# Optimization experiments

Hardware: AMD Instinct MI355X
Metric: run time of the kernel (lower is better)

The kernel has to match this reference:

```python
import jax, jax.numpy as jnp
import numpy as np

D_MODEL = 256
NUM_HEADS = 8
HEAD_DIM = D_MODEL // NUM_HEADS


def setup_inputs() -> dict:
    key = jax.random.key(0)
    ks = jax.random.split(key, 16)
    B, C, H, W = 2, D_MODEL, 64, 64
    s = 0.02
    inp = {
        "query_feat": jax.random.normal(ks[0], (B, C, H, W), jnp.float32),
        "lateral_feat": jax.random.normal(ks[1], (B, C, H, W), jnp.float32),
        # 1x1 convs == per-pixel linear layers: weight (out, in), bias (out,)
        "Wq": jax.random.normal(ks[2], (C, C), jnp.float32) * s,
        "bq": jnp.zeros((C,), jnp.float32),
        "Wk": jax.random.normal(ks[3], (C, C), jnp.float32) * s,
        "bk": jnp.zeros((C,), jnp.float32),
        "Wv": jax.random.normal(ks[4], (C, C), jnp.float32) * s,
        "bv": jnp.zeros((C,), jnp.float32),
        "Wo": jax.random.normal(ks[5], (C, C), jnp.float32) * s,
        "bo": jnp.zeros((C,), jnp.float32),
        "W1": jax.random.normal(ks[6], (4 * C, C), jnp.float32) * s,
        "b1": jnp.zeros((4 * C,), jnp.float32),
        "W2": jax.random.normal(ks[7], (C, 4 * C), jnp.float32) * s,
        "b2": jnp.zeros((C,), jnp.float32),
    }
    return inp


def reference(query_feat, lateral_feat, Wq, bq, Wk, bk, Wv, bv, Wo, bo, W1, b1, W2, b2):
    B, C, H, W = query_feat.shape
    N = H * W
    h, d = NUM_HEADS, HEAD_DIM
    scale = d ** -0.5

    # (B,C,H,W) -> (B,N,C) tokens
    xq = query_feat.reshape(B, C, N).transpose(0, 2, 1)
    xl = lateral_feat.reshape(B, C, N).transpose(0, 2, 1)

    # 1x1-conv projections = dense per-token linear
    Q = (xq @ Wq.T + bq).reshape(B, N, h, d).transpose(0, 2, 1, 3)  # (B,h,N,d)
    K = (xl @ Wk.T + bk).reshape(B, N, h, d).transpose(0, 2, 1, 3)
    V = (xl @ Wv.T + bv).reshape(B, N, h, d).transpose(0, 2, 1, 3)

    scores = jnp.einsum("bhqd,bhkd->bhqk", Q, K) * scale  # (B,h,N,N)
    attn = jax.nn.softmax(scores, axis=-1)  # dropout = identity at inference
    out = jnp.einsum("bhqk,bhkd->bhqd", attn, V)  # (B,h,N,d)

    out = out.transpose(0, 2, 1, 3).reshape(B, N, C)  # (B,N,C)
    out = out @ Wo.T + bo
    out = out.transpose(0, 2, 1).reshape(B, C, H, W)
    out = out + query_feat  # residual

    # MLP on channels (1x1 convs + exact GELU)
    t = out.reshape(B, C, N).transpose(0, 2, 1)  # (B,N,C)
    hdn = jax.nn.gelu(t @ W1.T + b1, approximate=False)  # (B,N,4C)
    mlp = (hdn @ W2.T + b2).transpose(0, 2, 1).reshape(B, C, H, W)
    return out + mlp
```

## Files before the change

### kernel.cpp

```cpp
#include <hip/hip_runtime.h>
#include <math.h>

namespace {

constexpr int kB  = 2;
constexpr int kC  = 256;
constexpr int kN  = 4096;
constexpr int kHD = 32;
constexpr int kC4 = 1024;

typedef __attribute__((ext_vector_type(8))) short bf16x8;
typedef __attribute__((ext_vector_type(4))) float f32x4;
typedef __attribute__((ext_vector_type(16))) float f32x16;

__device__ __forceinline__ float gelu_exact(float x) {
  return 0.5f * x * (1.0f + erff(x * 0.70710678118654752f));
}

__device__ __forceinline__ unsigned short f2bf(float x) {
  unsigned u = __builtin_bit_cast(unsigned, x);
  u += 0x7FFFu + ((u >> 16) & 1u);
  return (unsigned short)(u >> 16);
}

__device__ __forceinline__ float bf2f(unsigned short us) {
  return __builtin_bit_cast(float, (unsigned)us << 16);
}

__device__ __forceinline__ float exp2_hw(float x) {
#if __has_builtin(__builtin_amdgcn_exp2f)
  return __builtin_amdgcn_exp2f(x);
#else
  float r;
  asm("v_exp_f32 %0, %1\n\ts_nop 1" : "=v"(r) : "v"(x));
  return r;
#endif
}

__device__ __forceinline__ unsigned cvt_pk_bf16(float lo, float hi) {
  unsigned r;
  asm("v_cvt_pk_bf16_f32 %0, %1, %2" : "=v"(r) : "v"(lo), "v"(hi));
  return r;
}

__global__ __launch_bounds__(256)
void convert_all(const float* __restrict__ qfeat, const float* __restrict__ lfeat,
                 const float* __restrict__ Wq, const float* __restrict__ Wk,
                 const float* __restrict__ Wv, const float* __restrict__ Wo,
                 const float* __restrict__ W1, const float* __restrict__ W2,
                 unsigned short* __restrict__ qtok, unsigned short* __restrict__ ltok,
                 unsigned short* __restrict__ wbf)
{
  __shared__ float Lds[32][36];
  const int z = blockIdx.z;
  const int t = threadIdx.x;
  if (z < 4) {
    const float* src = (z < kB) ? qfeat : lfeat;
    unsigned short* dst = (z < kB) ? qtok : ltok;
    const int b = z & 1;
    src += (size_t)b * kC * kN;
    dst += (size_t)b * kN * kC;
    const int n0 = blockIdx.x * 32, c0 = blockIdx.y * 32;
    const int r = t >> 3, q4 = (t & 7) * 4;
    {
      const float4 v = *(const float4*)&src[(size_t)(c0 + r) * kN + n0 + q4];
      Lds[r][q4 + 0] = v.x; Lds[r][q4 + 1] = v.y; Lds[r][q4 + 2] = v.z; Lds[r][q4 + 3] = v.w;
    }
    __syncthreads();
    ushort4 p;
    p.x = f2bf(Lds[q4 + 0][r]); p.y = f2bf(Lds[q4 + 1][r]);
    p.z = f2bf(Lds[q4 + 2][r]); p.w = f2bf(Lds[q4 + 3][r]);
    *(ushort4*)&dst[(size_t)(n0 + r) * kC + c0 + q4] = p;
  } else {
    const int wi = blockIdx.y * 128 + blockIdx.x;
    if (wi >= 768) return;
    const int i4 = wi * 1024 + t * 4;
    const float* s; int base;
    if      (i4 < 65536)  { s = Wq; base = 0; }
    else if (i4 < 131072) { s = Wk; base = 65536; }
    else if (i4 < 196608) { s = Wv; base = 131072; }
    else if (i4 < 262144) { s = Wo; base = 196608; }
    else if (i4 < 524288) { s = W1; base = 262144; }
    else                  { s = W2; base = 524288; }
    const float4 v = *(const float4*)&s[i4 - base];
    ushort4 p;
    p.x = f2bf(v.x); p.y = f2bf(v.y); p.z = f2bf(v.z); p.w = f2bf(v.w);
    *(ushort4*)&wbf[i4] = p;
  }
}

template <int EPI, bool GELU, bool RES>
__global__ __launch_bounds__(256)
void gemm_mfma(const unsigned short* __restrict__ Wbf,
               const unsigned short* __restrict__ Xtok,
               const float* __restrict__ bias, const float* __restrict__ res,
               void* __restrict__ Y1, void* __restrict__ Y2,
               int M, int Nn, int K, float oscale)
{
  __shared__ unsigned short Wlds[64 * 64];
  __shared__ unsigned short Xlds[64 * 64];

  const int z = blockIdx.z;
  Xtok += (size_t)z * Nn * K;

  const int t = threadIdx.x;
  const int w = t >> 6, l = t & 63;
  const int r = l & 15, g = l >> 4;
  const int wm = w >> 1, wn = w & 1;
  const int m0 = blockIdx.y * 64, n0 = blockIdx.x * 64;

  const int rw = t >> 3;
  const int sw = (t & 7) ^ (rw & 7);
  const unsigned short* wsrc = Wbf + (size_t)(m0 + rw) * K + sw * 8;
  const unsigned short* xsrc = Xtok + (size_t)(n0 + rw) * K + sw * 8;

  f32x4 acc[2][2];
#pragma unroll
  for (int i = 0; i < 2; ++i)
#pragma unroll
    for (int j = 0; j < 2; ++j) acc[i][j] = {0.f, 0.f, 0.f, 0.f};

  bf16x8 wrg[2], xrg[2];
#pragma unroll
  for (int j = 0; j < 2; ++j) {
    wrg[j] = *(const bf16x8*)(wsrc + (size_t)(32 * j) * K);
    xrg[j] = *(const bf16x8*)(xsrc + (size_t)(32 * j) * K);
  }

  for (int k0 = 0; k0 < K; k0 += 64) {
    __syncthreads();
    *(bf16x8*)((char*)Wlds + t * 16)         = wrg[0];
    *(bf16x8*)((char*)Wlds + (256 + t) * 16) = wrg[1];
    *(bf16x8*)((char*)Xlds + t * 16)         = xrg[0];
    *(bf16x8*)((char*)Xlds + (256 + t) * 16) = xrg[1];
    __syncthreads();
    if (k0 + 64 < K) {
#pragma unroll
      for (int j = 0; j < 2; ++j) {
        wrg[j] = *(const bf16x8*)(wsrc + (size_t)(32 * j) * K + k0 + 64);
        xrg[j] = *(const bf16x8*)(xsrc + (size_t)(32 * j) * K + k0 + 64);
      }
    }
#pragma unroll
    for (int kc = 0; kc < 2; ++kc) {
      const int sl = ((kc * 4 + g) ^ (r & 7)) * 16;
      bf16x8 a0 = *(const bf16x8*)((const char*)Wlds + (wm * 32 + r) * 128 + sl);
      bf16x8 a1 = *(const bf16x8*)((const char*)Wlds + (wm * 32 + 16 + r) * 128 + sl);
      bf16x8 b0 = *(const bf16x8*)((const char*)Xlds + (wn * 32 + r) * 128 + sl);
      bf16x8 b1 = *(const bf16x8*)((const char*)Xlds + (wn * 32 + 16 + r) * 128 + sl);
      acc[0][0] = __builtin_amdgcn_mfma_f32_16x16x32_bf16(a0, b0, acc[0][0], 0, 0, 0);
      acc[0][1] = __builtin_amdgcn_mfma_f32_16x16x32_bf16(a0, b1, acc[0][1], 0, 0, 0);
      acc[1][0] = __builtin_amdgcn_mfma_f32_16x16x32_bf16(a1, b0, acc[1][0], 0, 0, 0);
      acc[1][1] = __builtin_amdgcn_mfma_f32_16x16x32_bf16(a1, b1, acc[1][1], 0, 0, 0);
    }
  }

#pragma unroll
  for (int f = 0; f < 2; ++f) {
    const int mb = m0 + wm * 32 + f * 16 + 4 * g;
    const float* bp = bias + mb;
    if constexpr (EPI == 4) { if (mb >= (M >> 1)) bp = res + (mb - (M >> 1)); }
    const float4 b4 = *(const float4*)bp;
#pragma unroll
    for (int fn = 0; fn < 2; ++fn) {
      const int n = n0 + wn * 32 + fn * 16 + r;
      float v[4];
      v[0] = (acc[f][fn][0] + b4.x) * oscale; v[1] = (acc[f][fn][1] + b4.y) * oscale;
      v[2] = (acc[f][fn][2] + b4.z) * oscale; v[3] = (acc[f][fn][3] + b4.w) * oscale;
      if (GELU) {
#pragma unroll
        for (int q = 0; q < 4; ++q) v[q] = gelu_exact(v[q]);
      }
      if (RES) {
#pragma unroll
        for (int q = 0; q < 4; ++q)
          v[q] += res[(size_t)z * M * Nn + (size_t)(mb + q) * Nn + n];
      }
      if constexpr (EPI == 1) {
        unsigned short* Yt = (unsigned short*)Y1 + (size_t)z * Nn * M;
        ushort4 pk;
        pk.x = f2bf(v[0]); pk.y = f2bf(v[1]); pk.z = f2bf(v[2]); pk.w = f2bf(v[3]);
        *(ushort4*)&Yt[(size_t)n * M + mb] = pk;
      }
      if constexpr (EPI == 4) {
        const int Mh = M >> 1;
        if (mb < Mh) {
          unsigned short* Yt = (unsigned short*)Y1 + (size_t)z * Nn * Mh;
          ushort4 pk;
          pk.x = f2bf(v[0]); pk.y = f2bf(v[1]); pk.z = f2bf(v[2]); pk.w = f2bf(v[3]);
          *(ushort4*)&Yt[(size_t)n * Mh + mb] = pk;
        } else {
          unsigned short* Yc = (unsigned short*)Y2 + (size_t)z * Mh * Nn;
#pragma unroll
          for (int q = 0; q < 4; ++q) Yc[(size_t)(mb - Mh + q) * Nn + n] = f2bf(v[q]);
        }
      }
      if constexpr (EPI == 6) {
        float* Yf = (float*)Y1 + (size_t)z * M * Nn;
        const unsigned short* Rt = (const unsigned short*)Y2 + (size_t)z * Nn * M;
#pragma unroll
        for (int q = 0; q < 4; ++q)
          Yf[(size_t)(mb + q) * Nn + n] = v[q] + bf2f(Rt[(size_t)n * M + mb + q]);
      }
    }
  }
}

__global__ __launch_bounds__(512, 4)
void attn_mfma32(const unsigned short* __restrict__ Qbf,
                 const unsigned short* __restrict__ Kbf,
                 const unsigned short* __restrict__ Vbf,
                 unsigned short* __restrict__ Aout)
{
  __shared__ __attribute__((aligned(16))) char smem[32768];

  const int id = blockIdx.x;
  const int bh = id & 15;
  const int b = bh >> 3, hd = bh & 7;
  const int t = threadIdx.x;
  const int w = t >> 6, l = t & 63;
  const int r = l & 31, hi = l >> 5;
  const int qg = w >> 1, kh = w & 1;

  const unsigned short* Qb = Qbf + (size_t)b * kN * kC;
  const unsigned short* Kb = Kbf + (size_t)b * kN * kC;
  const unsigned short* Vb = Vbf + ((size_t)b * kC + hd * kHD) * kN;
  unsigned short* Ap = Aout + (size_t)b * kN * kC;

  const int q0 = (id >> 4) * 128 + qg * 32;

  const bf16x8 qf0 = *(const bf16x8*)&Qb[(size_t)(q0 + r) * kC + hd * kHD + hi * 8];
  const bf16x8 qf1 = *(const bf16x8*)&Qb[(size_t)(q0 + r) * kC + hd * kHD + 16 + hi * 8];

  const int tt = t & 255, th = t >> 8;
  const unsigned short* ksrc = Kb + (size_t)(th * 2048 + (tt >> 2)) * kC + hd * kHD + (tt & 3) * 8;
  const unsigned short* vsrc = Vb + (size_t)(tt >> 3) * kN + th * 2048 + (tt & 7) * 8;
  char* kdst = smem + th * 4096 + ((tt & 3) * 64 + ((tt >> 2) ^ (9 * (tt & 3)))) * 16;
  char* vdst = smem + 8192 + th * 4096 + ((tt & 7) * 32 + ((tt >> 3) ^ (tt & 7))) * 16;

  int koff[2][2], voff[2][2];
#pragma unroll
  for (int ds = 0; ds < 2; ++ds)
#pragma unroll
    for (int tile = 0; tile < 2; ++tile) {
      const int c = 2 * ds + hi;
      koff[ds][tile] = kh * 4096 + (c * 64 + tile * 32 + (r ^ (9 * c))) * 16;
    }
#pragma unroll
  for (int ktile = 0; ktile < 2; ++ktile)
#pragma unroll
    for (int kc = 0; kc < 2; ++kc) {
      const int c = ktile * 4 + kc * 2 + hi;
      voff[ktile][kc] = 8192 + kh * 4096 + (c * 32 + (r ^ c)) * 16;
    }

  const f32x16 ZV = {0.f};
  f32x16 oA = ZV, oB = ZV;
  float lsum = 0.f;

  bf16x8 krg = *(const bf16x8*)ksrc;
  bf16x8 vrg = *(const bf16x8*)vsrc;

  for (int it = 0; it < 32; ++it) {
    const int bo = (it & 1) << 14;
    *(bf16x8*)(kdst + bo) = krg;
    *(bf16x8*)(vdst + bo) = vrg;
    if (it + 1 < 32) {
      krg = *(const bf16x8*)(ksrc + (size_t)(it + 1) * 64 * kC);
      vrg = *(const bf16x8*)(vsrc + (it + 1) * 64);
    }
    __syncthreads();

    bf16x8 ka00 = *(const bf16x8*)(smem + bo + koff[0][0]);
    bf16x8 ka10 = *(const bf16x8*)(smem + bo + koff[1][0]);
    bf16x8 ka01 = *(const bf16x8*)(smem + bo + koff[0][1]);
    bf16x8 ka11 = *(const bf16x8*)(smem + bo + koff[1][1]);
    __builtin_amdgcn_s_setprio(1);
    f32x16 s0 = __builtin_amdgcn_mfma_f32_32x32x16_bf16(ka00, qf0, ZV, 0, 0, 0);
    s0        = __builtin_amdgcn_mfma_f32_32x32x16_bf16(ka10, qf1, s0, 0, 0, 0);
    f32x16 s1 = __builtin_amdgcn_mfma_f32_32x32x16_bf16(ka01, qf0, ZV, 0, 0, 0);
    s1        = __builtin_amdgcn_mfma_f32_32x32x16_bf16(ka11, qf1, s1, 0, 0, 0);
    __builtin_amdgcn_s_setprio(0);

#pragma unroll
    for (int ktile = 0; ktile < 2; ++ktile) {
      const f32x16& sv = ktile ? s1 : s0;
      float pe[16];
#pragma unroll
      for (int j = 0; j < 16; ++j) pe[j] = exp2_hw(sv[j]);
      lsum += (((pe[0] + pe[1]) + (pe[2] + pe[3])) + ((pe[4] + pe[5]) + (pe[6] + pe[7])))
            + (((pe[8] + pe[9]) + (pe[10] + pe[11])) + ((pe[12] + pe[13]) + (pe[14] + pe[15])));
      const unsigned c0 = cvt_pk_bf16(pe[0], pe[1]),   c1 = cvt_pk_bf16(pe[2], pe[3]);
      const unsigned c2 = cvt_pk_bf16(pe[4], pe[5]),   c3 = cvt_pk_bf16(pe[6], pe[7]);
      const unsigned c4 = cvt_pk_bf16(pe[8], pe[9]),   c5 = cvt_pk_bf16(pe[10], pe[11]);
      const unsigned c6 = cvt_pk_bf16(pe[12], pe[13]), c7 = cvt_pk_bf16(pe[14], pe[15]);
      auto a02 = __builtin_amdgcn_permlane32_swap(c0, c2, false, false);
      auto a13 = __builtin_amdgcn_permlane32_swap(c1, c3, false, false);
      auto a46 = __builtin_amdgcn_permlane32_swap(c4, c6, false, false);
      auto a57 = __builtin_amdgcn_permlane32_swap(c5, c7, false, false);
      union { unsigned u[4]; bf16x8 v; } p0, p1;
      p0.u[0] = a02[0]; p0.u[1] = a13[0]; p0.u[2] = a02[1]; p0.u[3] = a13[1];
      p1.u[0] = a46[0]; p1.u[1] = a57[0]; p1.u[2] = a46[1]; p1.u[3] = a57[1];
      bf16x8 vf0 = *(const bf16x8*)(smem + bo + voff[ktile][0]);
      bf16x8 vf1 = *(const bf16x8*)(smem + bo + voff[ktile][1]);
      __builtin_amdgcn_s_setprio(1);
      oA = __builtin_amdgcn_mfma_f32_32x32x16_bf16(vf0, p0.v, oA, 0, 0, 0);
      oB = __builtin_amdgcn_mfma_f32_32x32x16_bf16(vf1, p1.v, oB, 0, 0, 0);
      __builtin_amdgcn_s_setprio(0);
    }
  }

  {
    auto pr = __builtin_amdgcn_permlane32_swap(
        __builtin_bit_cast(unsigned, lsum), __builtin_bit_cast(unsigned, lsum), false, false);
    lsum = __builtin_bit_cast(float, (unsigned)pr[0]) + __builtin_bit_cast(float, (unsigned)pr[1]);
  }
  float oS[16];
#pragma unroll
  for (int j = 0; j < 16; ++j) oS[j] = oA[j] + oB[j];

  float* Scr = (float*)smem;
  __syncthreads();
  if (kh == 1) {
    float* S = Scr + ((size_t)qg * 64 + l) * 17;
#pragma unroll
    for (int j = 0; j < 16; ++j) S[j] = oS[j];
    S[16] = lsum;
  }
  __syncthreads();
  if (kh == 0) {
    const float* S = Scr + ((size_t)qg * 64 + l) * 17;
#pragma unroll
    for (int j = 0; j < 16; ++j) oS[j] += S[j];
    lsum += S[16];
    const float inv = 1.f / lsum;

    unsigned* T = (unsigned*)(Scr + (size_t)qg * 64 * 17);
#pragma unroll
    for (int p = 0; p < 8; ++p) {
      const int r2 = 4 * (p >> 1) + 2 * hi + (p & 1);
      T[r2 * 33 + r] = cvt_pk_bf16(oS[2 * p] * inv, oS[2 * p + 1] * inv);
    }
    unsigned v[8];
#pragma unroll
    for (int j = 0; j < 8; ++j) v[j] = T[(8 * hi + j) * 33 + r];
    unsigned short* outp = Ap + (size_t)(q0 + r) * kC + hd * kHD + hi * 16;
    uint4 w0{v[0], v[1], v[2], v[3]}, w1{v[4], v[5], v[6], v[7]};
    *(uint4*)outp = w0;
    *(uint4*)(outp + 8) = w1;
  }
}

}

extern "C" void kernel_launch(void* const* d_in, const int* in_sizes, int n_in,
                              void* d_out, int out_size, void* d_ws, size_t ws_size,
                              hipStream_t stream)
{
  const float* qfeat = (const float*)d_in[0];
  const float* lfeat = (const float*)d_in[1];
  const float* Wq = (const float*)d_in[2];
  const float* bq = (const float*)d_in[3];
  const float* Wk = (const float*)d_in[4];
  const float* bk = (const float*)d_in[5];
  const float* Wv = (const float*)d_in[6];
  const float* bv = (const float*)d_in[7];
  const float* Wo = (const float*)d_in[8];
  const float* bo = (const float*)d_in[9];
  const float* W1 = (const float*)d_in[10];
  const float* b1 = (const float*)d_in[11];
  const float* W2 = (const float*)d_in[12];
  const float* b2 = (const float*)d_in[13];
  float* out = (float*)d_out;
  (void)in_sizes; (void)n_in; (void)out_size; (void)ws_size;

  constexpr float kScaleLog2e = 0.25506970f;

  const size_t bcn = (size_t)kB * kC * kN;
  unsigned short* qtok   = (unsigned short*)d_ws;
  unsigned short* ltok   = qtok + bcn;
  unsigned short* wbf    = ltok + bcn;
  unsigned short* qbf    = wbf + 786432;
  unsigned short* kbf    = qbf + bcn;
  unsigned short* vbf    = kbf + bcn;
  unsigned short* atok   = vbf + bcn;
  unsigned short* owstok = atok + bcn;
  unsigned short* h1tok  = owstok + bcn;

  dim3 blk(256);

  convert_all<<<dim3(128, 8, 5), blk, 0, stream>>>(
      qfeat, lfeat, Wq, Wk, Wv, Wo, W1, W2, qtok, ltok, wbf);

  gemm_mfma<1, false, false><<<dim3(64, 4, 2), blk, 0, stream>>>(
      wbf, qtok, bq, nullptr, qbf, nullptr, kC, kN, kC, kScaleLog2e);
  gemm_mfma<4, false, false><<<dim3(64, 8, 2), blk, 0, stream>>>(
      wbf + 65536, ltok, bk, bv, kbf, vbf, 2 * kC, kN, kC, 1.0f);

  attn_mfma32<<<dim3(512), dim3(512), 0, stream>>>(qbf, kbf, vbf, atok);

  gemm_mfma<1, false, true><<<dim3(64, 4, 2), blk, 0, stream>>>(
      wbf + 196608, atok, bo, qfeat, owstok, nullptr, kC, kN, kC, 1.0f);
  gemm_mfma<1, true, false><<<dim3(64, 16, 2), blk, 0, stream>>>(
      wbf + 262144, owstok, b1, nullptr, h1tok, nullptr, kC4, kN, kC, 1.0f);
  gemm_mfma<6, false, false><<<dim3(64, 4, 2), blk, 0, stream>>>(
      wbf + 524288, h1tok, b2, nullptr, out, owstok, kC, kN, kC4, 1.0f);
}
```

Measured before the change: 103.7 us.

## Software-pipeline attention loop: overlap next QK MFMA with current softmax-PV

The attention inner loop is restructured so that the QK^T MFMA for the next key tile is issued before the exp/PV work for the current tile, using two sets of score accumulators and a 4-stage LDS ring (LDS grows from 32KB to 64KB). The goal is to hide exp and permlane latency behind matrix-core work. The cost is higher register pressure from the extra score tiles, and the doubled shared memory may cut how many blocks fit per CU under the launch bound of 4.

```diff
diff --git a/kernel.cpp b/kernel.cpp
--- a/kernel.cpp
+++ b/kernel.cpp
@@ -212,7 +212,7 @@
                  const unsigned short* __restrict__ Vbf,
                  unsigned short* __restrict__ Aout)
 {
-  __shared__ __attribute__((aligned(16))) char smem[32768];
+  __shared__ __attribute__((aligned(16))) char smem[65536];
 
   const int id = blockIdx.x;
   const int bh = id & 15;
@@ -258,33 +258,27 @@
   f32x16 oA = ZV, oB = ZV;
   float lsum = 0.f;
 
-  bf16x8 krg = *(const bf16x8*)ksrc;
-  bf16x8 vrg = *(const bf16x8*)vsrc;
-
-  for (int it = 0; it < 32; ++it) {
-    const int bo = (it & 1) << 14;
-    *(bf16x8*)(kdst + bo) = krg;
-    *(bf16x8*)(vdst + bo) = vrg;
-    if (it + 1 < 32) {
-      krg = *(const bf16x8*)(ksrc + (size_t)(it + 1) * 64 * kC);
-      vrg = *(const bf16x8*)(vsrc + (it + 1) * 64);
-    }
-    __syncthreads();
-
+  auto smfma = [&](f32x16& d0, f32x16& d1, int bo) {
     bf16x8 ka00 = *(const bf16x8*)(smem + bo + koff[0][0]);
     bf16x8 ka10 = *(const bf16x8*)(smem + bo + koff[1][0]);
     bf16x8 ka01 = *(const bf16x8*)(smem + bo + koff[0][1]);
     bf16x8 ka11 = *(const bf16x8*)(smem + bo + koff[1][1]);
     __builtin_amdgcn_s_setprio(1);
-    f32x16 s0 = __builtin_amdgcn_mfma_f32_32x32x16_bf16(ka00, qf0, ZV, 0, 0, 0);
-    s0        = __builtin_amdgcn_mfma_f32_32x32x16_bf16(ka10, qf1, s0, 0, 0, 0);
-    f32x16 s1 = __builtin_amdgcn_mfma_f32_32x32x16_bf16(ka01, qf0, ZV, 0, 0, 0);
-    s1        = __builtin_amdgcn_mfma_f32_32x32x16_bf16(ka11, qf1, s1, 0, 0, 0);
+    d0 = __builtin_amdgcn_mfma_f32_32x32x16_bf16(ka00, qf0, ZV, 0, 0, 0);
+    d0 = __builtin_amdgcn_mfma_f32_32x32x16_bf16(ka10, qf1, d0, 0, 0, 0);
+    d1 = __builtin_amdgcn_mfma_f32_32x32x16_bf16(ka01, qf0, ZV, 0, 0, 0);
+    d1 = __builtin_amdgcn_mfma_f32_32x32x16_bf16(ka11, qf1, d1, 0, 0, 0);
     __builtin_amdgcn_s_setprio(0);
-
+  };
+
+  auto softmax_pv = [&](const f32x16& s0v, const f32x16& s1v, int bo) {
+    bf16x8 vf00 = *(const bf16x8*)(smem + bo + voff[0][0]);
+    bf16x8 vf01 = *(const bf16x8*)(smem + bo + voff[0][1]);
+    bf16x8 vf10 = *(const bf16x8*)(smem + bo + voff[1][0]);
+    bf16x8 vf11 = *(const bf16x8*)(smem + bo + voff[1][1]);
 #pragma unroll
     for (int ktile = 0; ktile < 2; ++ktile) {
-      const f32x16& sv = ktile ? s1 : s0;
+      const f32x16& sv = ktile ? s1v : s0v;
       float pe[16];
 #pragma unroll
       for (int j = 0; j < 16; ++j) pe[j] = exp2_hw(sv[j]);
@@ -301,14 +295,63 @@
       union { unsigned u[4]; bf16x8 v; } p0, p1;
       p0.u[0] = a02[0]; p0.u[1] = a13[0]; p0.u[2] = a02[1]; p0.u[3] = a13[1];
       p1.u[0] = a46[0]; p1.u[1] = a57[0]; p1.u[2] = a46[1]; p1.u[3] = a57[1];
-      bf16x8 vf0 = *(const bf16x8*)(smem + bo + voff[ktile][0]);
-      bf16x8 vf1 = *(const bf16x8*)(smem + bo + voff[ktile][1]);
       __builtin_amdgcn_s_setprio(1);
-      oA = __builtin_amdgcn_mfma_f32_32x32x16_bf16(vf0, p0.v, oA, 0, 0, 0);
-      oB = __builtin_amdgcn_mfma_f32_32x32x16_bf16(vf1, p1.v, oB, 0, 0, 0);
+      oA = __builtin_amdgcn_mfma_f32_32x32x16_bf16(ktile ? vf10 : vf00, p0.v, oA, 0, 0, 0);
+      oB = __builtin_amdgcn_mfma_f32_32x32x16_bf16(ktile ? vf11 : vf01, p1.v, oB, 0, 0, 0);
       __builtin_amdgcn_s_setprio(0);
     }
-  }
+  };
+
+  f32x16 sA0, sA1, sB0, sB1;
+  bf16x8 krgE, vrgE, krgO, vrgO;
+
+  krgE = *(const bf16x8*)ksrc;
+  vrgE = *(const bf16x8*)vsrc;
+  *(bf16x8*)kdst = krgE;
+  *(bf16x8*)vdst = vrgE;
+  krgO = *(const bf16x8*)(ksrc + (size_t)64 * kC);
+  vrgO = *(const bf16x8*)(vsrc + 64);
+  __syncthreads();
+  smfma(sA0, sA1, 0);
+
+  const unsigned short* kload = ksrc + (size_t)128 * kC;
+  const unsigned short* vload = vsrc + 128;
+
+  for (int u = 0; u < 15; ++u) {
+    const int te = 2 * u;
+    {
+      const int bw = ((te + 1) & 3) << 14, br = (te & 3) << 14;
+      *(bf16x8*)(kdst + bw) = krgO;
+      *(bf16x8*)(vdst + bw) = vrgO;
+      krgE = *(const bf16x8*)kload;
+      vrgE = *(const bf16x8*)vload;
+      kload += (size_t)64 * kC; vload += 64;
+      __syncthreads();
+      smfma(sB0, sB1, bw);
+      softmax_pv(sA0, sA1, br);
+    }
+    {
+      const int to = te + 1;
+      const int bw = ((to + 1) & 3) << 14, br = (to & 3) << 14;
+      *(bf16x8*)(kdst + bw) = krgE;
+      *(bf16x8*)(vdst + bw) = vrgE;
+      krgO = *(const bf16x8*)kload;
+      vrgO = *(const bf16x8*)vload;
+      kload += (size_t)64 * kC; vload += 64;
+      __syncthreads();
+      smfma(sA0, sA1, bw);
+      softmax_pv(sB0, sB1, br);
+    }
+  }
+  {
+    const int bw = 3 << 14, br = 2 << 14;
+    *(bf16x8*)(kdst + bw) = krgO;
+    *(bf16x8*)(vdst + bw) = vrgO;
+    __syncthreads();
+    smfma(sB0, sB1, bw);
+    softmax_pv(sA0, sA1, br);
+  }
+  softmax_pv(sB0, sB1, 3 << 14);
 
   {
     auto pr = __builtin_amdgcn_permlane32_swap(
```

New measurement: 286.3 us. 2.76x slower.

## Double-buffer GEMM LDS tiles, merge Q/K/V projections, read residual from bf16 tokens

Applied to the files above, without the earlier changes.

Both GEMM kernels now keep two LDS buffers, so each iteration needs one barrier instead of two and the next tile's global loads overlap the current MFMA work. The Q and K/V projection GEMMs are merged into one launch (gemm_qkv), which removes a kernel launch and fills the GPU with a single larger grid. The output-projection residual is now read as coalesced bf16 from the token-major qtok buffer instead of strided fp32 from qfeat. That residual is rounded to bf16 before being added, which costs a little accuracy.

```diff
diff --git a/kernel.cpp b/kernel.cpp
--- a/kernel.cpp
+++ b/kernel.cpp
@@ -89,6 +89,109 @@
   }
 }
 
+__global__ __launch_bounds__(256)
+void gemm_qkv(const unsigned short* __restrict__ wbf,
+              const unsigned short* __restrict__ qtok,
+              const unsigned short* __restrict__ ltok,
+              const float* __restrict__ bq, const float* __restrict__ bk,
+              const float* __restrict__ bv,
+              unsigned short* __restrict__ qout, unsigned short* __restrict__ kout,
+              unsigned short* __restrict__ vout, float qscale)
+{
+  __shared__ unsigned short Wlds[2][64 * 64];
+  __shared__ unsigned short Xlds[2][64 * 64];
+
+  const int z = blockIdx.z;
+  const bool isQ = blockIdx.y < 4;
+  const int m0 = (isQ ? blockIdx.y : blockIdx.y - 4) * 64;
+  const unsigned short* Wb = isQ ? wbf : (wbf + 65536);
+  const unsigned short* Xt = (isQ ? qtok : ltok) + (size_t)z * kN * kC;
+
+  const int t = threadIdx.x;
+  const int w = t >> 6, l = t & 63;
+  const int r = l & 15, g = l >> 4;
+  const int wm = w >> 1, wn = w & 1;
+  const int n0 = blockIdx.x * 64;
+
+  const int rw = t >> 3;
+  const int sw = (t & 7) ^ (rw & 7);
+  const unsigned short* wsrc = Wb + (size_t)(m0 + rw) * kC + sw * 8;
+  const unsigned short* xsrc = Xt + (size_t)(n0 + rw) * kC + sw * 8;
+
+  f32x4 acc[2][2];
+#pragma unroll
+  for (int i = 0; i < 2; ++i)
+#pragma unroll
+    for (int j = 0; j < 2; ++j) acc[i][j] = {0.f, 0.f, 0.f, 0.f};
+
+  bf16x8 wrg[2], xrg[2];
+#pragma unroll
+  for (int j = 0; j < 2; ++j) {
+    wrg[j] = *(const bf16x8*)(wsrc + (size_t)(32 * j) * kC);
+    xrg[j] = *(const bf16x8*)(xsrc + (size_t)(32 * j) * kC);
+  }
+
+  for (int it = 0; it < 4; ++it) {
+    unsigned short* wl = &Wlds[it & 1][0];
+    unsigned short* xl = &Xlds[it & 1][0];
+    *(bf16x8*)((char*)wl + t * 16)         = wrg[0];
+    *(bf16x8*)((char*)wl + (256 + t) * 16) = wrg[1];
+    *(bf16x8*)((char*)xl + t * 16)         = xrg[0];
+    *(bf16x8*)((char*)xl + (256 + t) * 16) = xrg[1];
+    if (it + 1 < 4) {
+      const int ko = (it + 1) * 64;
+#pragma unroll
+      for (int j = 0; j < 2; ++j) {
+        wrg[j] = *(const bf16x8*)(wsrc + (size_t)(32 * j) * kC + ko);
+        xrg[j] = *(const bf16x8*)(xsrc + (size_t)(32 * j) * kC + ko);
+      }
+    }
+    __syncthreads();
+#pragma unroll
+    for (int kc = 0; kc < 2; ++kc) {
+      const int sl = ((kc * 4 + g) ^ (r & 7)) * 16;
+      bf16x8 a0 = *(const bf16x8*)((const char*)wl + (wm * 32 + r) * 128 + sl);
+      bf16x8 a1 = *(const bf16x8*)((const char*)wl + (wm * 32 + 16 + r) * 128 + sl);
+      bf16x8 b0 = *(const bf16x8*)((const char*)xl + (wn * 32 + r) * 128 + sl);
+      bf16x8 b1 = *(const bf16x8*)((const char*)xl + (wn * 32 + 16 + r) * 128 + sl);
+      acc[0][0] = __builtin_amdgcn_mfma_f32_16x16x32_bf16(a0, b0, acc[0][0], 0, 0, 0);
+      acc[0][1] = __builtin_amdgcn_mfma_f32_16x16x32_bf16(a0, b1, acc[0][1], 0, 0, 0);
+      acc[1][0] = __builtin_amdgcn_mfma_f32_16x16x32_bf16(a1, b0, acc[1][0], 0, 0, 0);
+      acc[1][1] = __builtin_amdgcn_mfma_f32_16x16x32_bf16(a1, b1, acc[1][1], 0, 0, 0);
+    }
+  }
+
+#pragma unroll
+  for (int f = 0; f < 2; ++f) {
+    const int mb = m0 + wm * 32 + f * 16 + 4 * g;
+    const float* bp = isQ ? (bq + mb) : (mb < 256 ? (bk + mb) : (bv + mb - 256));
+    const float4 b4 = *(const float4*)bp;
+    const float os = isQ ? qscale : 1.0f;
+#pragma unroll
+    for (int fn = 0; fn < 2; ++fn) {
+      const int n = n0 + wn * 32 + fn * 16 + r;
+      float v[4];
+      v[0] = (acc[f][fn][0] + b4.x) * os; v[1] = (acc[f][fn][1] + b4.y) * os;
+      v[2] = (acc[f][fn][2] + b4.z) * os; v[3] = (acc[f][fn][3] + b4.w) * os;
+      if (isQ) {
+        unsigned short* Yt = qout + (size_t)z * kN * kC;
+        ushort4 pk;
+        pk.x = f2bf(v[0]); pk.y = f2bf(v[1]); pk.z = f2bf(v[2]); pk.w = f2bf(v[3]);
+        *(ushort4*)&Yt[(size_t)n * kC + mb] = pk;
+      } else if (mb < 256) {
+        unsigned short* Yt = kout + (size_t)z * kN * kC;
+        ushort4 pk;
+        pk.x = f2bf(v[0]); pk.y = f2bf(v[1]); pk.z = f2bf(v[2]); pk.w = f2bf(v[3]);
+        *(ushort4*)&Yt[(size_t)n * kC + mb] = pk;
+      } else {
+        unsigned short* Yc = vout + (size_t)z * kC * kN;
+#pragma unroll
+        for (int q = 0; q < 4; ++q) Yc[(size_t)(mb - 256 + q) * kN + n] = f2bf(v[q]);
+      }
+    }
+  }
+}
+
 template <int EPI, bool GELU, bool RES>
 __global__ __launch_bounds__(256)
 void gemm_mfma(const unsigned short* __restrict__ Wbf,
@@ -97,8 +200,8 @@
                void* __restrict__ Y1, void* __restrict__ Y2,
                int M, int Nn, int K, float oscale)
 {
-  __shared__ unsigned short Wlds[64 * 64];
-  __shared__ unsigned short Xlds[64 * 64];
+  __shared__ unsigned short Wlds[2][64 * 64];
+  __shared__ unsigned short Xlds[2][64 * 64];
 
   const int z = blockIdx.z;
   Xtok += (size_t)z * Nn * K;
@@ -127,27 +230,30 @@
     xrg[j] = *(const bf16x8*)(xsrc + (size_t)(32 * j) * K);
   }
 
-  for (int k0 = 0; k0 < K; k0 += 64) {
+  const int nit = K >> 6;
+  for (int it = 0; it < nit; ++it) {
+    unsigned short* wl = &Wlds[it & 1][0];
+    unsigned short* xl = &Xlds[it & 1][0];
+    *(bf16x8*)((char*)wl + t * 16)         = wrg[0];
+    *(bf16x8*)((char*)wl + (256 + t) * 16) = wrg[1];
+    *(bf16x8*)((char*)xl + t * 16)         = xrg[0];
+    *(bf16x8*)((char*)xl + (256 + t) * 16) = xrg[1];
+    if (it + 1 < nit) {
+      const int ko = (it + 1) * 64;
+#pragma unroll
+      for (int j = 0; j < 2; ++j) {
+        wrg[j] = *(const bf16x8*)(wsrc + (size_t)(32 * j) * K + ko);
+        xrg[j] = *(const bf16x8*)(xsrc + (size_t)(32 * j) * K + ko);
+      }
+    }
     __syncthreads();
-    *(bf16x8*)((char*)Wlds + t * 16)         = wrg[0];
-    *(bf16x8*)((char*)Wlds + (256 + t) * 16) = wrg[1];
-    *(bf16x8*)((char*)Xlds + t * 16)         = xrg[0];
-    *(bf16x8*)((char*)Xlds + (256 + t) * 16) = xrg[1];
-    __syncthreads();
-    if (k0 + 64 < K) {
-#pragma unroll
-      for (int j = 0; j < 2; ++j) {
-        wrg[j] = *(const bf16x8*)(wsrc + (size_t)(32 * j) * K + k0 + 64);
-        xrg[j] = *(const bf16x8*)(xsrc + (size_t)(32 * j) * K + k0 + 64);
-      }
-    }
 #pragma unroll
     for (int kc = 0; kc < 2; ++kc) {
       const int sl = ((kc * 4 + g) ^ (r & 7)) * 16;
-      bf16x8 a0 = *(const bf16x8*)((const char*)Wlds + (wm * 32 + r) * 128 + sl);
-      bf16x8 a1 = *(const bf16x8*)((const char*)Wlds + (wm * 32 + 16 + r) * 128 + sl);
-      bf16x8 b0 = *(const bf16x8*)((const char*)Xlds + (wn * 32 + r) * 128 + sl);
-      bf16x8 b1 = *(const bf16x8*)((const char*)Xlds + (wn * 32 + 16 + r) * 128 + sl);
+      bf16x8 a0 = *(const bf16x8*)((const char*)wl + (wm * 32 + r) * 128 + sl);
+      bf16x8 a1 = *(const bf16x8*)((const char*)wl + (wm * 32 + 16 + r) * 128 + sl);
+      bf16x8 b0 = *(const bf16x8*)((const char*)xl + (wn * 32 + r) * 128 + sl);
+      bf16x8 b1 = *(const bf16x8*)((const char*)xl + (wn * 32 + 16 + r) * 128 + sl);
       acc[0][0] = __builtin_amdgcn_mfma_f32_16x16x32_bf16(a0, b0, acc[0][0], 0, 0, 0);
       acc[0][1] = __builtin_amdgcn_mfma_f32_16x16x32_bf16(a0, b1, acc[0][1], 0, 0, 0);
       acc[1][0] = __builtin_amdgcn_mfma_f32_16x16x32_bf16(a1, b0, acc[1][0], 0, 0, 0);
@@ -158,9 +264,7 @@
 #pragma unroll
   for (int f = 0; f < 2; ++f) {
     const int mb = m0 + wm * 32 + f * 16 + 4 * g;
-    const float* bp = bias + mb;
-    if constexpr (EPI == 4) { if (mb >= (M >> 1)) bp = res + (mb - (M >> 1)); }
-    const float4 b4 = *(const float4*)bp;
+    const float4 b4 = *(const float4*)&bias[mb];
 #pragma unroll
     for (int fn = 0; fn < 2; ++fn) {
       const int n = n0 + wn * 32 + fn * 16 + r;
@@ -176,24 +280,16 @@
         for (int q = 0; q < 4; ++q)
           v[q] += res[(size_t)z * M * Nn + (size_t)(mb + q) * Nn + n];
       }
-      if constexpr (EPI == 1) {
+      if constexpr (EPI == 7) {
+        const unsigned short* Rt = (const unsigned short*)Y2 + (size_t)z * Nn * M;
+        const ushort4 rr = *(const ushort4*)&Rt[(size_t)n * M + mb];
+        v[0] += bf2f(rr.x); v[1] += bf2f(rr.y); v[2] += bf2f(rr.z); v[3] += bf2f(rr.w);
+      }
+      if constexpr (EPI == 1 || EPI == 7) {
         unsigned short* Yt = (unsigned short*)Y1 + (size_t)z * Nn * M;
         ushort4 pk;
         pk.x = f2bf(v[0]); pk.y = f2bf(v[1]); pk.z = f2bf(v[2]); pk.w = f2bf(v[3]);
         *(ushort4*)&Yt[(size_t)n * M + mb] = pk;
-      }
-      if constexpr (EPI == 4) {
-        const int Mh = M >> 1;
-        if (mb < Mh) {
-          unsigned short* Yt = (unsigned short*)Y1 + (size_t)z * Nn * Mh;
-          ushort4 pk;
-          pk.x = f2bf(v[0]); pk.y = f2bf(v[1]); pk.z = f2bf(v[2]); pk.w = f2bf(v[3]);
-          *(ushort4*)&Yt[(size_t)n * Mh + mb] = pk;
-        } else {
-          unsigned short* Yc = (unsigned short*)Y2 + (size_t)z * Mh * Nn;
-#pragma unroll
-          for (int q = 0; q < 4; ++q) Yc[(size_t)(mb - Mh + q) * Nn + n] = f2bf(v[q]);
-        }
       }
       if constexpr (EPI == 6) {
         float* Yf = (float*)Y1 + (size_t)z * M * Nn;
@@ -392,15 +488,13 @@
   convert_all<<<dim3(128, 8, 5), blk, 0, stream>>>(
       qfeat, lfeat, Wq, Wk, Wv, Wo, W1, W2, qtok, ltok, wbf);
 
-  gemm_mfma<1, false, false><<<dim3(64, 4, 2), blk, 0, stream>>>(
-      wbf, qtok, bq, nullptr, qbf, nullptr, kC, kN, kC, kScaleLog2e);
-  gemm_mfma<4, false, false><<<dim3(64, 8, 2), blk, 0, stream>>>(
-      wbf + 65536, ltok, bk, bv, kbf, vbf, 2 * kC, kN, kC, 1.0f);
+  gemm_qkv<<<dim3(64, 12, 2), blk, 0, stream>>>(
+      wbf, qtok, ltok, bq, bk, bv, qbf, kbf, vbf, kScaleLog2e);
 
   attn_mfma32<<<dim3(512), dim3(512), 0, stream>>>(qbf, kbf, vbf, atok);
 
-  gemm_mfma<1, false, true><<<dim3(64, 4, 2), blk, 0, stream>>>(
-      wbf + 196608, atok, bo, qfeat, owstok, nullptr, kC, kN, kC, 1.0f);
+  gemm_mfma<7, false, false><<<dim3(64, 4, 2), blk, 0, stream>>>(
+      wbf + 196608, atok, bo, nullptr, owstok, qtok, kC, kN, kC, 1.0f);
   gemm_mfma<1, true, false><<<dim3(64, 16, 2), blk, 0, stream>>>(
       wbf + 262144, owstok, b1, nullptr, h1tok, nullptr, kC4, kN, kC, 1.0f);
   gemm_mfma<6, false, false><<<dim3(64, 4, 2), blk, 0, stream>>>(
```

Result: faster. 100.0 us (median of 2 runs) (-3.5%).
